# Performance work log

Measured on AMD Instinct MI355X. Metric: run time of the kernel, lower is better.

Reference implementation:

```python
import jax, jax.numpy as jnp
import numpy as np

N_NODES = 50000
ALPHA_SLOPE = 0.2  # LeakyReLU negative slope
EPS = 1e-16


def setup_inputs() -> dict:
    key = jax.random.key(0)
    k1, k2, k3, k4 = jax.random.split(key, 4)
    in_features, heads, d = 512, 8, 32
    x = jax.random.normal(k1, (N_NODES, in_features), dtype=jnp.float32)
    edge_index = jax.random.randint(k2, (2, 800000), 0, N_NODES, dtype=jnp.int64)
    # xavier_normal with relu gain ~ sqrt(2) * sqrt(2/(fan_in+fan_out))
    w_std = np.sqrt(2.0) * np.sqrt(2.0 / (in_features + d))
    a_std = np.sqrt(2.0) * np.sqrt(2.0 / (1 + 2 * d))
    W = jax.random.normal(k3, (heads, in_features, d), dtype=jnp.float32) * w_std
    a = jax.random.normal(k4, (heads, 2 * d), dtype=jnp.float32) * a_std
    return {"x": x, "edge_index": edge_index, "W": W, "a": a}


def reference(x, edge_index, W, a):
    # x: [N, F_in], edge_index: [2, E], W: [H, F_in, D], a: [H, 2D]
    n = x.shape[0]
    d = W.shape[-1]
    e0, e1 = edge_index[0], edge_index[1]
    # per-head projected features: [N, H, D]
    h = jnp.einsum('nf,hfd->nhd', x, W)
    # attention logits: a.mm(cat(h[e0], h[e1]).T) == a_src.h[e0] + a_dst.h[e1]
    a_src, a_dst = a[:, :d], a[:, d:]          # [H, D] each
    s_src = jnp.einsum('nhd,hd->nh', h, a_src)  # [N, H]
    s_dst = jnp.einsum('nhd,hd->nh', h, a_dst)  # [N, H]
    logits = s_src[e0] + s_dst[e1]              # [E, H]
    logits = jnp.where(logits >= 0, logits, ALPHA_SLOPE * logits)  # LeakyReLU
    # segment softmax over destination node e0
    m = jax.ops.segment_max(logits, e0, num_segments=n)   # [N, H]
    ex = jnp.exp(logits - m[e0])                          # [E, H]
    denom = jax.ops.segment_sum(ex, e0, num_segments=n)   # [N, H]
    alpha = ex / (denom[e0] + EPS)                        # [E, H]
    # dropout is identity in eval mode
    # sparse aggregate: out[e0] += alpha * h[e1]
    msg = alpha[:, :, None] * h[e1]                       # [E, H, D]
    out = jax.ops.segment_sum(msg, e0, num_segments=n)    # [N, H, D]
    return out.reshape(n, -1)                             # concat heads -> [N, H*D]
```

## Files before the change

kernel.cpp:

```cpp
#include <hip/hip_runtime.h>

#define N_NODES 50000
#define N_EDGES 800000
#define IN_F    512
#define HEADS   8
#define DHEAD   32
#define NHD     256
#define SLOPE   0.2f
#define EPS_F   1e-16f
#define N_SBLK  ((N_NODES + 255) / 256)

typedef __attribute__((ext_vector_type(8))) short short8;
typedef __attribute__((ext_vector_type(4))) float f32x4;
typedef __attribute__((ext_vector_type(4))) unsigned short u16x4;

__device__ __forceinline__ unsigned short f2bf(float f) {
  unsigned int u = __float_as_uint(f);
  unsigned int r = u + 0x7FFFu + ((u >> 16) & 1u);
  return (unsigned short)(r >> 16);
}
__device__ __forceinline__ float bf2f(unsigned short s) {
  return __uint_as_float(((unsigned int)s) << 16);
}
__device__ __forceinline__ void gload_lds16(const void* g, void* l) {
  __builtin_amdgcn_global_load_lds((const __attribute__((address_space(1))) void*)g,
                                   (__attribute__((address_space(3))) void*)l, 16, 0, 0);
}

__global__ void k_cast_w(const float* __restrict__ W, unsigned short* __restrict__ WbT) {
  int id = blockIdx.x * blockDim.x + threadIdx.x;
  if (id >= NHD * IN_F) return;
  int c = id >> 9, k = id & 511;
  WbT[id] = f2bf(W[(c >> 5) * (IN_F * DHEAD) + k * DHEAD + (c & 31)]);
}

__global__ __launch_bounds__(256) void k_gemm_mfma(const float* __restrict__ x,
                                                   const unsigned short* __restrict__ WbT,
                                                   unsigned short* __restrict__ hb) {
  __shared__ unsigned short As[64 * 64];
  __shared__ unsigned short Bs[256 * 64];
  const int tid  = threadIdx.x;
  const int lane = tid & 63;
  const int wid  = tid >> 6;
  const int bm   = blockIdx.x * 64;
  const int wn   = wid * 64;

  const int arow = tid >> 3, ap = tid & 7, aq = ap ^ (arow & 7);
  const float* gA0 = x + (size_t)min(bm + arow,      N_NODES - 1) * IN_F + aq * 8;
  const float* gA1 = x + (size_t)min(bm + arow + 32, N_NODES - 1) * IN_F + aq * 8;
  unsigned short* lA0 = &As[(arow * 8 + ap) * 8];
  unsigned short* lA1 = &As[((arow + 32) * 8 + ap) * 8];

  const int bs = 512 * wid + lane;
  const int brow = bs >> 3, bp = bs & 7, bq = bp ^ (brow & 7);
  const unsigned short* gB = WbT + (size_t)brow * IN_F + bq * 8;
  unsigned short* lB = &Bs[(size_t)512 * wid * 8];

  f32x4 acc[4][4] = {};

  for (int k0 = 0; k0 < IN_F; k0 += 64) {
    __syncthreads();
#pragma unroll
    for (int it = 0; it < 8; ++it)
      gload_lds16(gB + k0 + it * 8 * IN_F, lB + it * 64 * 8);
    {
      float4 a00 = *(const float4*)(gA0 + k0);
      float4 a01 = *(const float4*)(gA0 + k0 + 4);
      float4 a10 = *(const float4*)(gA1 + k0);
      float4 a11 = *(const float4*)(gA1 + k0 + 4);
      short8 v0, v1;
      v0[0] = (short)f2bf(a00.x); v0[1] = (short)f2bf(a00.y);
      v0[2] = (short)f2bf(a00.z); v0[3] = (short)f2bf(a00.w);
      v0[4] = (short)f2bf(a01.x); v0[5] = (short)f2bf(a01.y);
      v0[6] = (short)f2bf(a01.z); v0[7] = (short)f2bf(a01.w);
      v1[0] = (short)f2bf(a10.x); v1[1] = (short)f2bf(a10.y);
      v1[2] = (short)f2bf(a10.z); v1[3] = (short)f2bf(a10.w);
      v1[4] = (short)f2bf(a11.x); v1[5] = (short)f2bf(a11.y);
      v1[6] = (short)f2bf(a11.z); v1[7] = (short)f2bf(a11.w);
      *(short8*)lA0 = v0;
      *(short8*)lA1 = v1;
    }
    __syncthreads();

#pragma unroll
    for (int kk = 0; kk < 2; ++kk) {
      short8 af[4], bfr[4];
#pragma unroll
      for (int i = 0; i < 4; ++i) {
        int r = i * 16 + (lane & 15);
        int q = kk * 4 + (lane >> 4);
        af[i] = *(const short8*)&As[(r * 8 + (q ^ (r & 7))) * 8];
      }
#pragma unroll
      for (int j = 0; j < 4; ++j) {
        int r = wn + j * 16 + (lane & 15);
        int q = kk * 4 + (lane >> 4);
        bfr[j] = *(const short8*)&Bs[(r * 8 + (q ^ (r & 7))) * 8];
      }
#pragma unroll
      for (int i = 0; i < 4; ++i)
#pragma unroll
        for (int j = 0; j < 4; ++j)
          acc[i][j] = __builtin_amdgcn_mfma_f32_16x16x32_bf16(af[i], bfr[j], acc[i][j], 0, 0, 0);
    }
  }

#pragma unroll
  for (int i = 0; i < 4; ++i) {
#pragma unroll
    for (int q = 0; q < 4; ++q) {
      int row = bm + i * 16 + (lane >> 4) * 4 + q;
      if (row < N_NODES) {
#pragma unroll
        for (int j = 0; j < 4; ++j)
          hb[(size_t)row * NHD + wn + j * 16 + (lane & 15)] = f2bf(acc[i][j][q]);
      }
    }
  }
}

__global__ __launch_bounds__(256) void k_scores(const unsigned short* __restrict__ hb,
                                                const float* __restrict__ a,
                                                float* __restrict__ s_src,
                                                float* __restrict__ s_dst) {
  int n = (blockIdx.x * blockDim.x + threadIdx.x) >> 6;
  int lane = threadIdx.x & 63;
  if (n >= N_NODES) return;
  int head = lane >> 3;
  int dofs = (lane & 7) * 4;
  u16x4 hv = *(const u16x4*)(hb + (size_t)n * NHD + lane * 4);
  float4 as = *(const float4*)(a + head * 2 * DHEAD + dofs);
  float4 ad = *(const float4*)(a + head * 2 * DHEAD + DHEAD + dofs);
  float h0 = bf2f(hv.x), h1 = bf2f(hv.y), h2 = bf2f(hv.z), h3 = bf2f(hv.w);
  float ss = h0 * as.x + h1 * as.y + h2 * as.z + h3 * as.w;
  float sd = h0 * ad.x + h1 * ad.y + h2 * ad.z + h3 * ad.w;
  ss += __shfl_xor(ss, 1); ss += __shfl_xor(ss, 2); ss += __shfl_xor(ss, 4);
  sd += __shfl_xor(sd, 1); sd += __shfl_xor(sd, 2); sd += __shfl_xor(sd, 4);
  if ((lane & 7) == 0) {
    s_src[n * 8 + head] = ss;
    s_dst[n * 8 + head] = sd;
  }
}

__global__ void k_hist(const int* __restrict__ ei, int* __restrict__ deg) {
  int e = blockIdx.x * blockDim.x + threadIdx.x;
  if (e < N_EDGES) atomicAdd(&deg[ei[e]], 1);
}

__global__ __launch_bounds__(256) void k_bsum(const int* __restrict__ deg,
                                              int* __restrict__ bsum) {
  __shared__ int sm[4];
  int i = blockIdx.x * 256 + threadIdx.x;
  int v = (i < N_NODES) ? deg[i] : 0;
#pragma unroll
  for (int o = 1; o < 64; o <<= 1) v += __shfl_xor(v, o);
  if ((threadIdx.x & 63) == 0) sm[threadIdx.x >> 6] = v;
  __syncthreads();
  if (threadIdx.x == 0) bsum[blockIdx.x] = sm[0] + sm[1] + sm[2] + sm[3];
}

__global__ __launch_bounds__(256) void k_scan_main(const int* __restrict__ deg,
                                                   const int* __restrict__ bsum,
                                                   int* __restrict__ rowptr,
                                                   int* __restrict__ cursor) {
  __shared__ int sb[256];
  __shared__ int sm[256];
  const int t = threadIdx.x;
  const int b = blockIdx.x;
  int bv = (t < N_SBLK) ? bsum[t] : 0;
  sb[t] = bv;
  int i = b * 256 + t;
  int v = (i < N_NODES) ? deg[i] : 0;
  sm[t] = v;
  __syncthreads();
#pragma unroll
  for (int o = 1; o < 256; o <<= 1) {
    int u1 = (t >= o) ? sb[t - o] : 0;
    int u2 = (t >= o) ? sm[t - o] : 0;
    __syncthreads();
    sb[t] += u1;
    sm[t] += u2;
    __syncthreads();
  }
  int boff = (b > 0) ? sb[b - 1] : 0;
  if (i < N_NODES) {
    int ex = boff + sm[t] - v;
    rowptr[i] = ex;
    cursor[i] = ex;
  }
  if (b == 0 && t == 0) rowptr[N_NODES] = sb[255];
}

__global__ void k_fill(const int* __restrict__ ei, int* __restrict__ cursor,
                       int* __restrict__ edst) {
  int e = blockIdx.x * blockDim.x + threadIdx.x;
  if (e >= N_EDGES) return;
  int p = atomicAdd(&cursor[ei[e]], 1);
  edst[p] = ei[N_EDGES + e];
}

__global__ __launch_bounds__(256) void k_aggr(const int* __restrict__ rowptr,
                                              const int* __restrict__ edst,
                                              const float* __restrict__ s_src,
                                              const float* __restrict__ s_dst,
                                              const unsigned short* __restrict__ hb,
                                              float* __restrict__ out) {
  int n = (int)((blockIdx.x * blockDim.x + threadIdx.x) >> 6);
  if (n >= N_NODES) return;
  n = __builtin_amdgcn_readfirstlane(n);
  const int lane = threadIdx.x & 63;
  const int head = lane >> 3;
  const float ssrc = s_src[n * 8 + head];
  int i = rowptr[n];
  const int iend = rowptr[n + 1];
  float den = 0.f;
  f32x4 acc = {0.f, 0.f, 0.f, 0.f};
  for (; i + 1 < iend; i += 2) {
    int d0 = edst[i], d1 = edst[i + 1];
    float v0 = ssrc + s_dst[d0 * 8 + head];
    float v1 = ssrc + s_dst[d1 * 8 + head];
    u16x4 h0 = *(const u16x4*)(hb + (size_t)d0 * NHD + lane * 4);
    u16x4 h1 = *(const u16x4*)(hb + (size_t)d1 * NHD + lane * 4);
    v0 = v0 >= 0.f ? v0 : SLOPE * v0;
    v1 = v1 >= 0.f ? v1 : SLOPE * v1;
    float e0 = __expf(v0), e1 = __expf(v1);
    den += e0 + e1;
    acc.x += e0 * bf2f(h0.x) + e1 * bf2f(h1.x);
    acc.y += e0 * bf2f(h0.y) + e1 * bf2f(h1.y);
    acc.z += e0 * bf2f(h0.z) + e1 * bf2f(h1.z);
    acc.w += e0 * bf2f(h0.w) + e1 * bf2f(h1.w);
  }
  if (i < iend) {
    int d0 = edst[i];
    float v0 = ssrc + s_dst[d0 * 8 + head];
    v0 = v0 >= 0.f ? v0 : SLOPE * v0;
    float e0 = __expf(v0);
    u16x4 h0 = *(const u16x4*)(hb + (size_t)d0 * NHD + lane * 4);
    den += e0;
    acc.x += e0 * bf2f(h0.x);
    acc.y += e0 * bf2f(h0.y);
    acc.z += e0 * bf2f(h0.z);
    acc.w += e0 * bf2f(h0.w);
  }
  float inv = 1.f / (den + EPS_F);
  *(f32x4*)(out + (size_t)n * NHD + lane * 4) = acc * inv;
}

extern "C" void kernel_launch(void* const* d_in, const int* in_sizes, int n_in,
                              void* d_out, int out_size, void* d_ws, size_t ws_size,
                              hipStream_t stream) {
  const float* x  = (const float*)d_in[0];
  const int*   ei = (const int*)d_in[1];
  const float* W  = (const float*)d_in[2];
  const float* a  = (const float*)d_in[3];
  float* out = (float*)d_out;

  unsigned short* hb  = (unsigned short*)d_ws;
  unsigned short* WbT = hb + (size_t)N_NODES * NHD;
  float* s_src = (float*)(WbT + (size_t)NHD * IN_F);
  float* s_dst = s_src + (size_t)N_NODES * HEADS;
  int* deg    = (int*)(s_dst + (size_t)N_NODES * HEADS);
  int* cursor = deg + N_NODES;
  int* rowptr = cursor + N_NODES;
  int* bsum   = rowptr + 50008;
  int* edst   = bsum + 256;

  hipMemsetAsync(deg, 0, (size_t)N_NODES * sizeof(int), stream);
  k_cast_w<<<(NHD * IN_F + 255) / 256, 256, 0, stream>>>(W, WbT);
  k_gemm_mfma<<<(N_NODES + 63) / 64, 256, 0, stream>>>(x, WbT, hb);
  k_scores<<<(N_NODES * 64 + 255) / 256, 256, 0, stream>>>(hb, a, s_src, s_dst);
  k_hist<<<(N_EDGES + 255) / 256, 256, 0, stream>>>(ei, deg);
  k_bsum<<<N_SBLK, 256, 0, stream>>>(deg, bsum);
  k_scan_main<<<N_SBLK, 256, 0, stream>>>(deg, bsum, rowptr, cursor);
  k_fill<<<(N_EDGES + 255) / 256, 256, 0, stream>>>(ei, cursor, edst);
  k_aggr<<<(N_NODES * 64 + 255) / 256, 256, 0, stream>>>(rowptr, edst, s_src, s_dst, hb, out);
}
```

Baseline: 204.2 us.

## Fuse score computation and degree histogram into GEMM kernel, drop memset

Computes the per-node source and destination attention scores in the GEMM epilogue from fp32 accumulators using wave shuffles, which removes the separate k_scores pass that re-read the bf16 projected features. The degree histogram moves into extra blocks appended to the GEMM grid, so it runs alongside the GEMM tiles. Zeroing of deg moves into the weight-cast kernel, replacing the memset. Together this removes three launches and one full read of h. The scores are now taken from unrounded fp32 values, which changes numerics slightly, and the histogram blocks compete with GEMM blocks for compute units.

```diff
diff --git a/kernel.cpp b/kernel.cpp
--- a/kernel.cpp
+++ b/kernel.cpp
@@ -9,6 +9,8 @@
 #define SLOPE   0.2f
 #define EPS_F   1e-16f
 #define N_SBLK  ((N_NODES + 255) / 256)
+#define NB_GEMM ((N_NODES + 63) / 64)
+#define NB_HIST ((N_EDGES + 4095) / 4096)
 
 typedef __attribute__((ext_vector_type(8))) short short8;
 typedef __attribute__((ext_vector_type(4))) float f32x4;
@@ -27,16 +29,32 @@
                                    (__attribute__((address_space(3))) void*)l, 16, 0, 0);
 }
 
-__global__ void k_cast_w(const float* __restrict__ W, unsigned short* __restrict__ WbT) {
+__global__ void k_cast_w(const float* __restrict__ W, unsigned short* __restrict__ WbT,
+                         int* __restrict__ deg) {
   int id = blockIdx.x * blockDim.x + threadIdx.x;
-  if (id >= NHD * IN_F) return;
-  int c = id >> 9, k = id & 511;
-  WbT[id] = f2bf(W[(c >> 5) * (IN_F * DHEAD) + k * DHEAD + (c & 31)]);
+  if (id < NHD * IN_F) {
+    int c = id >> 9, k = id & 511;
+    WbT[id] = f2bf(W[(c >> 5) * (IN_F * DHEAD) + k * DHEAD + (c & 31)]);
+  }
+  if (id < N_NODES) deg[id] = 0;
 }
 
 __global__ __launch_bounds__(256) void k_gemm_mfma(const float* __restrict__ x,
                                                    const unsigned short* __restrict__ WbT,
-                                                   unsigned short* __restrict__ hb) {
+                                                   unsigned short* __restrict__ hb,
+                                                   const float* __restrict__ a,
+                                                   float* __restrict__ s_src,
+                                                   float* __restrict__ s_dst,
+                                                   const int* __restrict__ ei,
+                                                   int* __restrict__ deg) {
+  if (blockIdx.x >= NB_GEMM) {
+    int b = blockIdx.x - NB_GEMM;
+    int end = min(b * 4096 + 4096, N_EDGES);
+    for (int e = b * 4096 + threadIdx.x; e < end; e += 256)
+      atomicAdd(&deg[ei[e]], 1);
+    return;
+  }
+
   __shared__ unsigned short As[64 * 64];
   __shared__ unsigned short Bs[256 * 64];
   const int tid  = threadIdx.x;
@@ -105,46 +123,42 @@
     }
   }
 
+  const int h0 = 2 * wid, h1 = 2 * wid + 1;
+  const int dl = lane & 15;
+  const float as00 = a[h0 * 64 + dl],      as01 = a[h0 * 64 + 16 + dl];
+  const float as10 = a[h1 * 64 + dl],      as11 = a[h1 * 64 + 16 + dl];
+  const float ad00 = a[h0 * 64 + 32 + dl], ad01 = a[h0 * 64 + 48 + dl];
+  const float ad10 = a[h1 * 64 + 32 + dl], ad11 = a[h1 * 64 + 48 + dl];
+
 #pragma unroll
   for (int i = 0; i < 4; ++i) {
 #pragma unroll
     for (int q = 0; q < 4; ++q) {
       int row = bm + i * 16 + (lane >> 4) * 4 + q;
+      float ss0 = acc[i][0][q] * as00 + acc[i][1][q] * as01;
+      float ss1 = acc[i][2][q] * as10 + acc[i][3][q] * as11;
+      float sd0 = acc[i][0][q] * ad00 + acc[i][1][q] * ad01;
+      float sd1 = acc[i][2][q] * ad10 + acc[i][3][q] * ad11;
+#pragma unroll
+      for (int o = 1; o < 16; o <<= 1) {
+        ss0 += __shfl_xor(ss0, o);
+        ss1 += __shfl_xor(ss1, o);
+        sd0 += __shfl_xor(sd0, o);
+        sd1 += __shfl_xor(sd1, o);
+      }
       if (row < N_NODES) {
 #pragma unroll
         for (int j = 0; j < 4; ++j)
-          hb[(size_t)row * NHD + wn + j * 16 + (lane & 15)] = f2bf(acc[i][j][q]);
+          hb[(size_t)row * NHD + wn + j * 16 + dl] = f2bf(acc[i][j][q]);
+        if (dl == 0) {
+          s_src[row * 8 + h0] = ss0;
+          s_src[row * 8 + h1] = ss1;
+          s_dst[row * 8 + h0] = sd0;
+          s_dst[row * 8 + h1] = sd1;
+        }
       }
     }
   }
-}
-
-__global__ __launch_bounds__(256) void k_scores(const unsigned short* __restrict__ hb,
-                                                const float* __restrict__ a,
-                                                float* __restrict__ s_src,
-                                                float* __restrict__ s_dst) {
-  int n = (blockIdx.x * blockDim.x + threadIdx.x) >> 6;
-  int lane = threadIdx.x & 63;
-  if (n >= N_NODES) return;
-  int head = lane >> 3;
-  int dofs = (lane & 7) * 4;
-  u16x4 hv = *(const u16x4*)(hb + (size_t)n * NHD + lane * 4);
-  float4 as = *(const float4*)(a + head * 2 * DHEAD + dofs);
-  float4 ad = *(const float4*)(a + head * 2 * DHEAD + DHEAD + dofs);
-  float h0 = bf2f(hv.x), h1 = bf2f(hv.y), h2 = bf2f(hv.z), h3 = bf2f(hv.w);
-  float ss = h0 * as.x + h1 * as.y + h2 * as.z + h3 * as.w;
-  float sd = h0 * ad.x + h1 * ad.y + h2 * ad.z + h3 * ad.w;
-  ss += __shfl_xor(ss, 1); ss += __shfl_xor(ss, 2); ss += __shfl_xor(ss, 4);
-  sd += __shfl_xor(sd, 1); sd += __shfl_xor(sd, 2); sd += __shfl_xor(sd, 4);
-  if ((lane & 7) == 0) {
-    s_src[n * 8 + head] = ss;
-    s_dst[n * 8 + head] = sd;
-  }
-}
-
-__global__ void k_hist(const int* __restrict__ ei, int* __restrict__ deg) {
-  int e = blockIdx.x * blockDim.x + threadIdx.x;
-  if (e < N_EDGES) atomicAdd(&deg[ei[e]], 1);
 }
 
 __global__ __launch_bounds__(256) void k_bsum(const int* __restrict__ deg,
@@ -265,11 +279,8 @@
   int* bsum   = rowptr + 50008;
   int* edst   = bsum + 256;
 
-  hipMemsetAsync(deg, 0, (size_t)N_NODES * sizeof(int), stream);
-  k_cast_w<<<(NHD * IN_F + 255) / 256, 256, 0, stream>>>(W, WbT);
-  k_gemm_mfma<<<(N_NODES + 63) / 64, 256, 0, stream>>>(x, WbT, hb);
-  k_scores<<<(N_NODES * 64 + 255) / 256, 256, 0, stream>>>(hb, a, s_src, s_dst);
-  k_hist<<<(N_EDGES + 255) / 256, 256, 0, stream>>>(ei, deg);
+  k_cast_w<<<512, 256, 0, stream>>>(W, WbT, deg);
+  k_gemm_mfma<<<NB_GEMM + NB_HIST, 256, 0, stream>>>(x, WbT, hb, a, s_src, s_dst, ei, deg);
   k_bsum<<<N_SBLK, 256, 0, stream>>>(deg, bsum);
   k_scan_main<<<N_SBLK, 256, 0, stream>>>(deg, bsum, rowptr, cursor);
   k_fill<<<(N_EDGES + 255) / 256, 256, 0, stream>>>(ei, cursor, edst);
```

New measurement: 192.0 us. 1.06x faster.
